# Performance work log

Hardware: AMD Instinct MI355X
Metric: run time of the kernel (lower is better)

The kernel has to match this reference:

```python
import jax, jax.numpy as jnp
import numpy as np

CHUNK = 1024  # rows of pc0 processed per tile to avoid materializing the full NxM matrix


def _min_sqdist(a, b):
    """For each row of a [N,3], min squared distance to rows of b [M,3]."""
    b_sq = jnp.sum(b * b, axis=1)  # [M]

    def tile_min(ac):  # ac: [CHUNK, 3]
        d = jnp.sum(ac * ac, axis=1)[:, None] + b_sq[None, :] - 2.0 * (ac @ b.T)
        return jnp.min(d, axis=1)

    n, dim = a.shape
    return jax.lax.map(tile_min, a.reshape(n // CHUNK, CHUNK, dim)).reshape(n)


def setup_inputs() -> dict:
    key = jax.random.key(0)
    k0, k1 = jax.random.split(key)
    pc0 = jax.random.normal(k0, (65536, 3), dtype=jnp.float32)
    pc1 = jax.random.normal(k1, (65536, 3), dtype=jnp.float32)
    return {"pc0": pc0, "pc1": pc1}


def reference(pc0, pc1):
    # chamfer forward: dist0[i] = min_j ||pc0[i]-pc1[j]||^2
    dist0 = _min_sqdist(pc0, pc1)
    mask = dist0 <= 2.0
    # mean over selected elements (boolean mask is constant wrt grads, as in torch)
    return jnp.sum(jnp.where(mask, dist0, 0.0)) / jnp.sum(mask).astype(dist0.dtype)
```

## Files before the change

### kernel.cpp

```cpp
#include <hip/hip_runtime.h>


constexpr int   NPTS  = 65536;
constexpr int   G     = 64;
constexpr int   NC    = G * G * G;
constexpr float H     = 0.125f;
constexpr float ORG   = -4.0f;
constexpr float INVH  = 8.0f;
constexpr int   G3    = 32;
constexpr float H3    = 0.25f;
constexpr float INVH3 = 4.0f;
constexpr int   BLOCK = 256;
constexpr int   PBLOCKS = 1024;
constexpr int   SB    = 128;
constexpr int   CHUNK = NC / SB;

__device__ __forceinline__ int cellOf(float x) {
  int c = (int)floorf((x - ORG) * INVH);
  return min(max(c, 0), G - 1);
}
__device__ __forceinline__ int cellOf3(float x) {
  int c = (int)floorf((x - ORG) * INVH3);
  return min(max(c, 0), G3 - 1);
}

__global__ __launch_bounds__(BLOCK) void count_kernel(
    const float* __restrict__ pc0, const float* __restrict__ pc1,
    unsigned* __restrict__ counts0, unsigned* __restrict__ counts1) {
  const int gid = blockIdx.x * BLOCK + threadIdx.x;
  const float* p; unsigned* cnt; int i;
  if (gid < NPTS) { p = pc1; cnt = counts1; i = gid; }
  else            { p = pc0; cnt = counts0; i = gid - NPTS; }
  const float x = p[3 * i], y = p[3 * i + 1], z = p[3 * i + 2];
  atomicAdd(&cnt[(cellOf(z) * G + cellOf(y)) * G + cellOf(x)], 1u);
}

__global__ __launch_bounds__(1024) void scan_partial_kernel(
    const unsigned* __restrict__ counts0, const unsigned* __restrict__ counts1,
    unsigned* __restrict__ partials) {
  const unsigned* counts = blockIdx.y ? counts0 : counts1;
  const int base = blockIdx.x * CHUNK + threadIdx.x * 2;
  unsigned sum = counts[base] + counts[base + 1];
  for (int o = 32; o; o >>= 1) sum += __shfl_down(sum, o, 64);
  __shared__ unsigned ws[16];
  if ((threadIdx.x & 63) == 0) ws[threadIdx.x >> 6] = sum;
  __syncthreads();
  if (threadIdx.x == 0) {
    unsigned t = 0;
    for (int w = 0; w < 16; ++w) t += ws[w];
    partials[blockIdx.y * SB + blockIdx.x] = t;
  }
}

__global__ __launch_bounds__(256) void scan_mid_kernel(
    unsigned* __restrict__ partials) {
  const int tid = threadIdx.x;
  const int g   = tid >> 7;
  const int li  = tid & 127;
  const unsigned v = partials[g * SB + li];
  unsigned inc = v;
  for (int o = 1; o < 64; o <<= 1) {
    const unsigned t = __shfl_up(inc, o, 64);
    if ((tid & 63) >= o) inc += t;
  }
  __shared__ unsigned wt[4];
  if ((tid & 63) == 63) wt[tid >> 6] = inc;
  __syncthreads();
  const unsigned woff = ((tid >> 6) & 1) ? wt[g << 1] : 0u;
  partials[g * SB + li] = woff + inc - v;
}

__global__ __launch_bounds__(1024) void scan_final_kernel(
    const unsigned* __restrict__ counts0, unsigned* __restrict__ cur0,
    const unsigned* __restrict__ counts1, unsigned* __restrict__ cur1,
    const unsigned* __restrict__ partials) {
  const unsigned* counts = blockIdx.y ? counts0 : counts1;
  unsigned* cur          = blockIdx.y ? cur0    : cur1;
  const int tid = threadIdx.x;
  const int base = blockIdx.x * CHUNK + tid * 2;
  const unsigned a = counts[base], b = counts[base + 1];
  const unsigned tsum = a + b;
  unsigned inc = tsum;
  for (int o = 1; o < 64; o <<= 1) {
    const unsigned t = __shfl_up(inc, o, 64);
    if ((tid & 63) >= o) inc += t;
  }
  __shared__ unsigned wt[16];
  if ((tid & 63) == 63) wt[tid >> 6] = inc;
  __syncthreads();
  if (tid < 16) {
    unsigned w = wt[tid];
    for (int o = 1; o < 16; o <<= 1) {
      const unsigned t = __shfl_up(w, o, 16);
      if (tid >= o) w += t;
    }
    wt[tid] = w;
  }
  __syncthreads();
  const unsigned woff = (tid >> 6) ? wt[(tid >> 6) - 1] : 0u;
  const unsigned off =
      partials[blockIdx.y * SB + blockIdx.x] + woff + inc - tsum;
  cur[base] = off;
  cur[base + 1] = off + a;
}

__global__ __launch_bounds__(BLOCK) void scatter_kernel(
    const float* __restrict__ pc0, const float* __restrict__ pc1,
    unsigned* __restrict__ cur0, unsigned* __restrict__ cur1,
    float4* __restrict__ q, float4* __restrict__ s) {
  const int gid = blockIdx.x * BLOCK + threadIdx.x;
  const float* p; unsigned* cur; float4* dst; int i;
  if (gid < NPTS) { p = pc1; cur = cur1; dst = s; i = gid; }
  else            { p = pc0; cur = cur0; dst = q; i = gid - NPTS; }
  const float x = p[3 * i], y = p[3 * i + 1], z = p[3 * i + 2];
  const int cid = (cellOf(z) * G + cellOf(y)) * G + cellOf(x);
  dst[atomicAdd(&cur[cid], 1u)] = make_float4(x, y, z, 0.f);
}

__global__ __launch_bounds__(BLOCK) void query_kernel(
    const float4* __restrict__ q, const unsigned* __restrict__ ends,
    const float4* __restrict__ s,
    unsigned* __restrict__ wl, float* __restrict__ wlBest,
    unsigned* __restrict__ pendCnt, float* __restrict__ bkt) {
  const int gtid = blockIdx.x * BLOCK + threadIdx.x;
  const int i   = gtid >> 2;
  const int sub = gtid & 3;
  const float4 p = q[i];
  const int cx = cellOf(p.x), cy = cellOf(p.y), cz = cellOf(p.z);
  const int x0 = max(cx - 1, 0), x1 = min(cx + 1, G - 1);

  unsigned rs[9], re[9];
#pragma unroll
  for (int rr = 0; rr < 9; ++rr) {
    const int zz = cz + rr / 3 - 1, yy = cy + rr % 3 - 1;
    const bool ok = (zz >= 0) && (zz < G) && (yy >= 0) && (yy < G);
    const int rb = ok ? (zz * G + yy) * G : 0;
    rs[rr] = ok ? ((rb + x0) ? ends[rb + x0 - 1] : 0u) : 0u;
    re[rr] = ok ? ends[rb + x1] : 0u;
  }
  float best = 3.4e38f;
#pragma unroll
  for (int rr = 0; rr < 9; ++rr) {
#pragma unroll 4
    for (unsigned j = rs[rr] + sub; j < re[rr]; j += 4) {
      const float4 c = s[j];
      const float dx = p.x - c.x, dy = p.y - c.y, dz = p.z - c.z;
      best = fminf(best, fmaf(dx, dx, fmaf(dy, dy, dz * dz)));
    }
  }
  best = fminf(best, __shfl_xor(best, 1, 64));
  best = fminf(best, __shfl_xor(best, 2, 64));

  float v = 0.f, c = 0.f;
  if (sub == 0) {
    const int y0 = max(cy - 1, 0), y1 = min(cy + 1, G - 1);
    const int z0 = max(cz - 1, 0), z1 = min(cz + 1, G - 1);
    const float dxl = (x0 == 0)     ? 1e9f : p.x - (ORG + (float)x0 * H);
    const float dxr = (x1 == G - 1) ? 1e9f : (ORG + (float)(x1 + 1) * H) - p.x;
    const float dyl = (y0 == 0)     ? 1e9f : p.y - (ORG + (float)y0 * H);
    const float dyr = (y1 == G - 1) ? 1e9f : (ORG + (float)(y1 + 1) * H) - p.y;
    const float dzl = (z0 == 0)     ? 1e9f : p.z - (ORG + (float)z0 * H);
    const float dzr = (z1 == G - 1) ? 1e9f : (ORG + (float)(z1 + 1) * H) - p.z;
    const float dbox = fminf(fminf(fminf(dxl, dxr), fminf(dyl, dyr)),
                             fminf(dzl, dzr));
    const float bnd2 = dbox * dbox * 0.999999f;
    if (best > bnd2) {
      const unsigned k = atomicAdd(pendCnt, 1u);
      wl[k] = (unsigned)i; wlBest[k] = best;
    } else if (best <= 2.0f) { v = best; c = 1.0f; }
  }

  for (int o = 32; o; o >>= 1) {
    v += __shfl_down(v, o, 64);
    c += __shfl_down(c, o, 64);
  }
  __shared__ float wsum[BLOCK / 64], wcnt[BLOCK / 64];
  const int wid = threadIdx.x >> 6;
  if ((threadIdx.x & 63) == 0) { wsum[wid] = v; wcnt[wid] = c; }
  __syncthreads();
  if (threadIdx.x == 0) {
    float bv = 0.f, bc = 0.f;
    for (int w = 0; w < BLOCK / 64; ++w) { bv += wsum[w]; bc += wcnt[w]; }
    if (bc != 0.f) {
      atomicAdd(&bkt[2 * (blockIdx.x & 63) + 0], bv);
      atomicAdd(&bkt[2 * (blockIdx.x & 63) + 1], bc);
    }
  }
}

__global__ __launch_bounds__(BLOCK) void pending_kernel(
    const float4* __restrict__ q,
    const unsigned* __restrict__ ends, const float4* __restrict__ s,
    const unsigned* __restrict__ wl, const float* __restrict__ wlBest,
    unsigned* __restrict__ pendCnt, float* __restrict__ bkt,
    unsigned* __restrict__ done, float* __restrict__ out) {
  __shared__ int snP;
  __shared__ float wsum[BLOCK / 64], wcnt[BLOCK / 64];
  __shared__ int isLast;
  __shared__ float fs[BLOCK / 64], fc[BLOCK / 64];
  if (threadIdx.x == 0) snP = (int)atomicAdd(pendCnt, 0u);
  __syncthreads();
  const int lane = threadIdx.x & 63, wid = threadIdx.x >> 6;
  const int gw = blockIdx.x * (BLOCK / 64) + wid;
  const int nW = PBLOCKS * (BLOCK / 64);
  float v = 0.f, c = 0.f;

  for (int it = gw; it < snP; it += nW) {
    const unsigned qi = wl[it];
    const float4 p = q[qi];
    const int cx = cellOf3(p.x), cy = cellOf3(p.y), cz = cellOf3(p.z);
    float best = wlBest[it];

    for (int r = 1; r <= 8; ++r) {
      const float cov = H3 * (float)(r - 1);
      if (best <= cov * cov) break;
      if (best > 2.0f && cov * cov >= 2.0f) break;
      const int S = (r == 1) ? 9 : 8 * r + 2 * (2 * r - 1) * (2 * r - 1);
      float b = best;
      for (int sI = lane; sI < S; sI += 64) {
        int dz, dy, xa, xb;
        if (r == 1) {
          dz = sI / 3 - 1; dy = sI % 3 - 1; xa = cx - 1; xb = cx + 1;
        } else if (sI < 8 * r) {
          if (sI < 2 * r + 1)      { dz = -r; dy = sI - r; }
          else if (sI < 4 * r + 2) { dz =  r; dy = sI - (2 * r + 1) - r; }
          else { const int t2 = sI - (4 * r + 2); dz = (t2 >> 1) - (r - 1);
                 dy = (t2 & 1) ? r : -r; }
          xa = cx - r; xb = cx + r;
        } else {
          const int t2 = sI - 8 * r, ci = t2 >> 1, w1 = 2 * r - 1;
          dz = ci / w1 - (r - 1); dy = ci % w1 - (r - 1);
          xa = xb = (t2 & 1) ? cx + r : cx - r;
        }
        const int Z = cz + dz, Y = cy + dy;
        if (Z < 0 || Z >= G3 || Y < 0 || Y >= G3) continue;
        int a3 = max(xa, 0), e3 = min(xb, G3 - 1);
        if (a3 > e3) continue;
        const float ylo = ORG + (float)Y * H3;
        const float zlo = ORG + (float)Z * H3;
        const float dyd = fmaxf(fmaxf(ylo - p.y, p.y - (ylo + H3)), 0.f);
        const float dzd = fmaxf(fmaxf(zlo - p.z, p.z - (zlo + H3)), 0.f);
        const float dyz2 = dyd * dyd + dzd * dzd;
        const float bnd = fminf(b, 2.0f);
        if (dyz2 >= bnd) continue;
        const float halfx = sqrtf(bnd - dyz2);
        const int xlo = (int)floorf((p.x - halfx - ORG) * INVH3);
        const int xhi = (int)floorf((p.x + halfx - ORG) * INVH3);
        a3 = max(a3, xlo); e3 = min(e3, xhi);
        if (a3 > e3) continue;
        const int xs = 2 * a3, xe = 2 * e3 + 1;
        unsigned js[4], je[4];
#pragma unroll
        for (int k = 0; k < 4; ++k) {
          const int zz = 2 * Z + (k >> 1), yy = 2 * Y + (k & 1);
          const int rb = (zz * G + yy) * G;
          js[k] = (rb + xs) ? ends[rb + xs - 1] : 0u;
          je[k] = ends[rb + xe];
        }
#pragma unroll
        for (int k = 0; k < 4; ++k) {
#pragma unroll 4
          for (unsigned j = js[k]; j < je[k]; ++j) {
            const float4 cd = s[j];
            const float dx = p.x - cd.x, dyv = p.y - cd.y, dzv = p.z - cd.z;
            b = fminf(b, fmaf(dx, dx, fmaf(dyv, dyv, dzv * dzv)));
          }
        }
      }
      for (int o = 32; o; o >>= 1) b = fminf(b, __shfl_xor(b, o, 64));
      best = b;
    }
    if (lane == 0 && best <= 2.0f) { v += best; c += 1.0f; }
  }

  if (lane == 0) { wsum[wid] = v; wcnt[wid] = c; }
  __syncthreads();
  if (threadIdx.x == 0) {
    float bv = 0.f, bc = 0.f;
    for (int w = 0; w < BLOCK / 64; ++w) { bv += wsum[w]; bc += wcnt[w]; }
    if (bc != 0.f) {
      atomicAdd(&bkt[2 * (blockIdx.x & 63) + 0], bv);
      atomicAdd(&bkt[2 * (blockIdx.x & 63) + 1], bc);
    }
    __threadfence();
    isLast = (atomicAdd(done, 1u) == (unsigned)(PBLOCKS - 1));
  }
  __syncthreads();
  if (isLast) {
    const float val = (threadIdx.x < 128) ? atomicAdd(&bkt[threadIdx.x], 0.0f) : 0.0f;
    float sv = (threadIdx.x & 1) ? 0.f : val;
    float cv = (threadIdx.x & 1) ? val : 0.f;
    for (int o = 32; o; o >>= 1) {
      sv += __shfl_down(sv, o, 64);
      cv += __shfl_down(cv, o, 64);
    }
    if (lane == 0) { fs[wid] = sv; fc[wid] = cv; }
    __syncthreads();
    if (threadIdx.x == 0) {
      float S = 0.f, C = 0.f;
      for (int w = 0; w < BLOCK / 64; ++w) { S += fs[w]; C += fc[w]; }
      out[0] = S / C;
    }
  }
}

extern "C" void kernel_launch(void* const* d_in, const int* in_sizes, int n_in,
                              void* d_out, int out_size, void* d_ws, size_t ws_size,
                              hipStream_t stream) {
  const float* pc0 = (const float*)d_in[0];
  const float* pc1 = (const float*)d_in[1];
  float* out = (float*)d_out;

  char* w = (char*)d_ws;
  auto nxt = [&](size_t bytes) {
    char* p = w; w += (bytes + 255) & ~(size_t)255; return p;
  };
  unsigned* counts1  = (unsigned*)nxt((size_t)NC * 4);
  unsigned* counts0  = (unsigned*)nxt((size_t)NC * 4);
  char*     misc     = nxt(1024);
  float*    bkt      = (float*)misc;
  unsigned* done     = (unsigned*)(misc + 512);
  unsigned* pendCnt  = (unsigned*)(misc + 516);
  unsigned* partials = (unsigned*)nxt((size_t)2 * SB * 4);
  unsigned* cur1     = (unsigned*)nxt((size_t)NC * 4);
  unsigned* cur0     = (unsigned*)nxt((size_t)NC * 4);
  float4*   s        = (float4*)nxt((size_t)NPTS * 16);
  float4*   q        = (float4*)nxt((size_t)NPTS * 16);
  unsigned* wl       = (unsigned*)nxt((size_t)NPTS * 4);
  float*    wlBest   = (float*)nxt((size_t)NPTS * 4);

  hipMemsetAsync(counts1, 0, (size_t)2 * NC * 4 + 1024, stream);

  count_kernel<<<2 * NPTS / BLOCK, BLOCK, 0, stream>>>(pc0, pc1, counts0, counts1);
  scan_partial_kernel<<<dim3(SB, 2), 1024, 0, stream>>>(counts0, counts1, partials);
  scan_mid_kernel<<<1, 256, 0, stream>>>(partials);
  scan_final_kernel<<<dim3(SB, 2), 1024, 0, stream>>>(counts0, cur0,
                                                      counts1, cur1, partials);
  scatter_kernel<<<2 * NPTS / BLOCK, BLOCK, 0, stream>>>(
      pc0, pc1, cur0, cur1, q, s);
  query_kernel<<<4 * NPTS / BLOCK, BLOCK, 0, stream>>>(q, cur1, s, wl, wlBest,
                                                       pendCnt, bkt);
  pending_kernel<<<PBLOCKS, BLOCK, 0, stream>>>(q, cur1, s, wl, wlBest,
                                                pendCnt, bkt, done, out);
}
```

Baseline: 136.6 us.

## Split each pending query's shell search across four wavefronts with atomic-min merge

Each pending query is now handled by four wavefronts instead of one. Each wavefront scans an interleaved quarter of the shell cells at every ring radius. Partial minima are merged with an atomicMin on the float's bit pattern, and the fourth wavefront to finish, detected through a per-query completion counter, adds the result to the masked sum. The aim is to cut the latency of long-running pending queries by adding parallelism, at the cost of extra atomics, a threadfence, a larger memset, and weaker early ring termination, since each subwave only sees its own running minimum.

```diff
diff --git a/kernel.cpp b/kernel.cpp
--- a/kernel.cpp
+++ b/kernel.cpp
@@ -12,6 +12,7 @@
 constexpr float INVH3 = 4.0f;
 constexpr int   BLOCK = 256;
 constexpr int   PBLOCKS = 1024;
+constexpr int   NSUB  = 4;
 constexpr int   SB    = 128;
 constexpr int   CHUNK = NC / SB;
 
@@ -26,8 +27,10 @@
 
 __global__ __launch_bounds__(BLOCK) void count_kernel(
     const float* __restrict__ pc0, const float* __restrict__ pc1,
-    unsigned* __restrict__ counts0, unsigned* __restrict__ counts1) {
+    unsigned* __restrict__ counts0, unsigned* __restrict__ counts1,
+    unsigned* __restrict__ pbestU) {
   const int gid = blockIdx.x * BLOCK + threadIdx.x;
+  if (gid < NPTS) pbestU[gid] = 0xFFFFFFFFu;
   const float* p; unsigned* cnt; int i;
   if (gid < NPTS) { p = pc1; cnt = counts1; i = gid; }
   else            { p = pc0; cnt = counts0; i = gid - NPTS; }
@@ -193,7 +196,8 @@
     const unsigned* __restrict__ ends, const float4* __restrict__ s,
     const unsigned* __restrict__ wl, const float* __restrict__ wlBest,
     unsigned* __restrict__ pendCnt, float* __restrict__ bkt,
-    unsigned* __restrict__ done, float* __restrict__ out) {
+    unsigned* __restrict__ done, float* __restrict__ out,
+    unsigned* __restrict__ pbestU, unsigned* __restrict__ pdone) {
   __shared__ int snP;
   __shared__ float wsum[BLOCK / 64], wcnt[BLOCK / 64];
   __shared__ int isLast;
@@ -205,7 +209,9 @@
   const int nW = PBLOCKS * (BLOCK / 64);
   float v = 0.f, c = 0.f;
 
-  for (int it = gw; it < snP; it += nW) {
+  for (int t = gw; t < snP * NSUB; t += nW) {
+    const int it  = t >> 2;
+    const int sw  = t & (NSUB - 1);
     const unsigned qi = wl[it];
     const float4 p = q[qi];
     const int cx = cellOf3(p.x), cy = cellOf3(p.y), cz = cellOf3(p.z);
@@ -217,7 +223,7 @@
       if (best > 2.0f && cov * cov >= 2.0f) break;
       const int S = (r == 1) ? 9 : 8 * r + 2 * (2 * r - 1) * (2 * r - 1);
       float b = best;
-      for (int sI = lane; sI < S; sI += 64) {
+      for (int sI = lane + (sw << 6); sI < S; sI += 64 * NSUB) {
         int dz, dy, xa, xb;
         if (r == 1) {
           dz = sI / 3 - 1; dy = sI % 3 - 1; xa = cx - 1; xb = cx + 1;
@@ -270,7 +276,14 @@
       for (int o = 32; o; o >>= 1) b = fminf(b, __shfl_xor(b, o, 64));
       best = b;
     }
-    if (lane == 0 && best <= 2.0f) { v += best; c += 1.0f; }
+    if (lane == 0) {
+      atomicMin(&pbestU[it], __float_as_uint(best));
+      __threadfence();
+      if (atomicAdd(&pdone[it], 1u) == NSUB - 1) {
+        const float fb = __uint_as_float(atomicAdd(&pbestU[it], 0u));
+        if (fb <= 2.0f) { v += fb; c += 1.0f; }
+      }
+    }
   }
 
   if (lane == 0) { wsum[wid] = v; wcnt[wid] = c; }
@@ -321,6 +334,7 @@
   float*    bkt      = (float*)misc;
   unsigned* done     = (unsigned*)(misc + 512);
   unsigned* pendCnt  = (unsigned*)(misc + 516);
+  unsigned* pdone    = (unsigned*)nxt((size_t)NPTS * 4);
   unsigned* partials = (unsigned*)nxt((size_t)2 * SB * 4);
   unsigned* cur1     = (unsigned*)nxt((size_t)NC * 4);
   unsigned* cur0     = (unsigned*)nxt((size_t)NC * 4);
@@ -328,10 +342,13 @@
   float4*   q        = (float4*)nxt((size_t)NPTS * 16);
   unsigned* wl       = (unsigned*)nxt((size_t)NPTS * 4);
   float*    wlBest   = (float*)nxt((size_t)NPTS * 4);
-
-  hipMemsetAsync(counts1, 0, (size_t)2 * NC * 4 + 1024, stream);
-
-  count_kernel<<<2 * NPTS / BLOCK, BLOCK, 0, stream>>>(pc0, pc1, counts0, counts1);
+  unsigned* pbestU   = (unsigned*)nxt((size_t)NPTS * 4);
+
+  hipMemsetAsync(counts1, 0, (size_t)2 * NC * 4 + 1024 + (size_t)NPTS * 4,
+                 stream);
+
+  count_kernel<<<2 * NPTS / BLOCK, BLOCK, 0, stream>>>(pc0, pc1, counts0,
+                                                       counts1, pbestU);
   scan_partial_kernel<<<dim3(SB, 2), 1024, 0, stream>>>(counts0, counts1, partials);
   scan_mid_kernel<<<1, 256, 0, stream>>>(partials);
   scan_final_kernel<<<dim3(SB, 2), 1024, 0, stream>>>(counts0, cur0,
@@ -341,5 +358,6 @@
   query_kernel<<<4 * NPTS / BLOCK, BLOCK, 0, stream>>>(q, cur1, s, wl, wlBest,
                                                        pendCnt, bkt);
   pending_kernel<<<PBLOCKS, BLOCK, 0, stream>>>(q, cur1, s, wl, wlBest,
-                                                pendCnt, bkt, done, out);
-}
+                                                pendCnt, bkt, done, out,
+                                                pbestU, pdone);
+}
```

New measurement: 348.7 us. 155% more time.

## Fuse query and pending kernels with a dynamic work-claiming queue

Applied to the files above, without the earlier changes.

Merges the first-pass query kernel and the pending-refinement kernel into one launch. Each block finishes its 3x3x3 cell query, publishes unresolved points to a worklist with fenced atomic writes, then its wavefronts claim worklist entries through an atomic counter. They spin with sleep until an entry is published or all query blocks are done. This removes a kernel launch and its tail gap, and lets refinement overlap with blocks still querying. In exchange it adds spin-wait polling, extra atomics, and a larger memset for the worklist tags.

```diff
diff --git a/kernel.cpp b/kernel.cpp
--- a/kernel.cpp
+++ b/kernel.cpp
@@ -11,7 +11,7 @@
 constexpr float H3    = 0.25f;
 constexpr float INVH3 = 4.0f;
 constexpr int   BLOCK = 256;
-constexpr int   PBLOCKS = 1024;
+constexpr int   NQB   = 4 * NPTS / BLOCK;
 constexpr int   SB    = 128;
 constexpr int   CHUNK = NC / SB;
 
@@ -117,99 +117,96 @@
   dst[atomicAdd(&cur[cid], 1u)] = make_float4(x, y, z, 0.f);
 }
 
-__global__ __launch_bounds__(BLOCK) void query_kernel(
+__global__ __launch_bounds__(BLOCK) void qp_kernel(
     const float4* __restrict__ q, const unsigned* __restrict__ ends,
     const float4* __restrict__ s,
-    unsigned* __restrict__ wl, float* __restrict__ wlBest,
-    unsigned* __restrict__ pendCnt, float* __restrict__ bkt) {
+    unsigned* __restrict__ wl, unsigned* __restrict__ wlBestU,
+    unsigned* __restrict__ pendCnt, unsigned* __restrict__ claim,
+    unsigned* __restrict__ qdone, float* __restrict__ bkt,
+    unsigned* __restrict__ done, float* __restrict__ out) {
   const int gtid = blockIdx.x * BLOCK + threadIdx.x;
-  const int i   = gtid >> 2;
-  const int sub = gtid & 3;
-  const float4 p = q[i];
-  const int cx = cellOf(p.x), cy = cellOf(p.y), cz = cellOf(p.z);
-  const int x0 = max(cx - 1, 0), x1 = min(cx + 1, G - 1);
-
-  unsigned rs[9], re[9];
+  const int lane = threadIdx.x & 63, wid = threadIdx.x >> 6;
+  float v = 0.f, c = 0.f;
+
+  {
+    const int i   = gtid >> 2;
+    const int sub = gtid & 3;
+    const float4 p = q[i];
+    const int cx = cellOf(p.x), cy = cellOf(p.y), cz = cellOf(p.z);
+    const int x0 = max(cx - 1, 0), x1 = min(cx + 1, G - 1);
+
+    unsigned rs[9], re[9];
 #pragma unroll
-  for (int rr = 0; rr < 9; ++rr) {
-    const int zz = cz + rr / 3 - 1, yy = cy + rr % 3 - 1;
-    const bool ok = (zz >= 0) && (zz < G) && (yy >= 0) && (yy < G);
-    const int rb = ok ? (zz * G + yy) * G : 0;
-    rs[rr] = ok ? ((rb + x0) ? ends[rb + x0 - 1] : 0u) : 0u;
-    re[rr] = ok ? ends[rb + x1] : 0u;
-  }
-  float best = 3.4e38f;
+    for (int rr = 0; rr < 9; ++rr) {
+      const int zz = cz + rr / 3 - 1, yy = cy + rr % 3 - 1;
+      const bool ok = (zz >= 0) && (zz < G) && (yy >= 0) && (yy < G);
+      const int rb = ok ? (zz * G + yy) * G : 0;
+      rs[rr] = ok ? ((rb + x0) ? ends[rb + x0 - 1] : 0u) : 0u;
+      re[rr] = ok ? ends[rb + x1] : 0u;
+    }
+    float best = 3.4e38f;
 #pragma unroll
-  for (int rr = 0; rr < 9; ++rr) {
+    for (int rr = 0; rr < 9; ++rr) {
 #pragma unroll 4
-    for (unsigned j = rs[rr] + sub; j < re[rr]; j += 4) {
-      const float4 c = s[j];
-      const float dx = p.x - c.x, dy = p.y - c.y, dz = p.z - c.z;
-      best = fminf(best, fmaf(dx, dx, fmaf(dy, dy, dz * dz)));
-    }
-  }
-  best = fminf(best, __shfl_xor(best, 1, 64));
-  best = fminf(best, __shfl_xor(best, 2, 64));
-
-  float v = 0.f, c = 0.f;
-  if (sub == 0) {
-    const int y0 = max(cy - 1, 0), y1 = min(cy + 1, G - 1);
-    const int z0 = max(cz - 1, 0), z1 = min(cz + 1, G - 1);
-    const float dxl = (x0 == 0)     ? 1e9f : p.x - (ORG + (float)x0 * H);
-    const float dxr = (x1 == G - 1) ? 1e9f : (ORG + (float)(x1 + 1) * H) - p.x;
-    const float dyl = (y0 == 0)     ? 1e9f : p.y - (ORG + (float)y0 * H);
-    const float dyr = (y1 == G - 1) ? 1e9f : (ORG + (float)(y1 + 1) * H) - p.y;
-    const float dzl = (z0 == 0)     ? 1e9f : p.z - (ORG + (float)z0 * H);
-    const float dzr = (z1 == G - 1) ? 1e9f : (ORG + (float)(z1 + 1) * H) - p.z;
-    const float dbox = fminf(fminf(fminf(dxl, dxr), fminf(dyl, dyr)),
-                             fminf(dzl, dzr));
-    const float bnd2 = dbox * dbox * 0.999999f;
-    if (best > bnd2) {
-      const unsigned k = atomicAdd(pendCnt, 1u);
-      wl[k] = (unsigned)i; wlBest[k] = best;
-    } else if (best <= 2.0f) { v = best; c = 1.0f; }
-  }
-
-  for (int o = 32; o; o >>= 1) {
-    v += __shfl_down(v, o, 64);
-    c += __shfl_down(c, o, 64);
-  }
-  __shared__ float wsum[BLOCK / 64], wcnt[BLOCK / 64];
-  const int wid = threadIdx.x >> 6;
-  if ((threadIdx.x & 63) == 0) { wsum[wid] = v; wcnt[wid] = c; }
-  __syncthreads();
-  if (threadIdx.x == 0) {
-    float bv = 0.f, bc = 0.f;
-    for (int w = 0; w < BLOCK / 64; ++w) { bv += wsum[w]; bc += wcnt[w]; }
-    if (bc != 0.f) {
-      atomicAdd(&bkt[2 * (blockIdx.x & 63) + 0], bv);
-      atomicAdd(&bkt[2 * (blockIdx.x & 63) + 1], bc);
-    }
-  }
-}
-
-__global__ __launch_bounds__(BLOCK) void pending_kernel(
-    const float4* __restrict__ q,
-    const unsigned* __restrict__ ends, const float4* __restrict__ s,
-    const unsigned* __restrict__ wl, const float* __restrict__ wlBest,
-    unsigned* __restrict__ pendCnt, float* __restrict__ bkt,
-    unsigned* __restrict__ done, float* __restrict__ out) {
-  __shared__ int snP;
-  __shared__ float wsum[BLOCK / 64], wcnt[BLOCK / 64];
-  __shared__ int isLast;
-  __shared__ float fs[BLOCK / 64], fc[BLOCK / 64];
-  if (threadIdx.x == 0) snP = (int)atomicAdd(pendCnt, 0u);
-  __syncthreads();
-  const int lane = threadIdx.x & 63, wid = threadIdx.x >> 6;
-  const int gw = blockIdx.x * (BLOCK / 64) + wid;
-  const int nW = PBLOCKS * (BLOCK / 64);
-  float v = 0.f, c = 0.f;
-
-  for (int it = gw; it < snP; it += nW) {
-    const unsigned qi = wl[it];
+      for (unsigned j = rs[rr] + sub; j < re[rr]; j += 4) {
+        const float4 cq = s[j];
+        const float dx = p.x - cq.x, dy = p.y - cq.y, dz = p.z - cq.z;
+        best = fminf(best, fmaf(dx, dx, fmaf(dy, dy, dz * dz)));
+      }
+    }
+    best = fminf(best, __shfl_xor(best, 1, 64));
+    best = fminf(best, __shfl_xor(best, 2, 64));
+
+    if (sub == 0) {
+      const int y0 = max(cy - 1, 0), y1 = min(cy + 1, G - 1);
+      const int z0 = max(cz - 1, 0), z1 = min(cz + 1, G - 1);
+      const float dxl = (x0 == 0)     ? 1e9f : p.x - (ORG + (float)x0 * H);
+      const float dxr = (x1 == G - 1) ? 1e9f : (ORG + (float)(x1 + 1) * H) - p.x;
+      const float dyl = (y0 == 0)     ? 1e9f : p.y - (ORG + (float)y0 * H);
+      const float dyr = (y1 == G - 1) ? 1e9f : (ORG + (float)(y1 + 1) * H) - p.y;
+      const float dzl = (z0 == 0)     ? 1e9f : p.z - (ORG + (float)z0 * H);
+      const float dzr = (z1 == G - 1) ? 1e9f : (ORG + (float)(z1 + 1) * H) - p.z;
+      const float dbox = fminf(fminf(fminf(dxl, dxr), fminf(dyl, dyr)),
+                               fminf(dzl, dzr));
+      const float bnd2 = dbox * dbox * 0.999999f;
+      if (best > bnd2) {
+        const unsigned k = atomicAdd(pendCnt, 1u);
+        atomicExch(&wlBestU[k], __float_as_uint(best));
+        __threadfence();
+        atomicExch(&wl[k], (unsigned)i + 1u);
+      } else if (best <= 2.0f) { v = best; c = 1.0f; }
+    }
+  }
+  __syncthreads();
+  if (threadIdx.x == 0) { __threadfence(); atomicAdd(qdone, 1u); }
+
+  for (;;) {
+    unsigned k = 0;
+    if (lane == 0) k = atomicAdd(claim, 1u);
+    k = __shfl(k, 0, 64);
+    if (k >= (unsigned)NPTS) break;
+    unsigned tag = 0;
+    if (lane == 0) {
+      int sp = 0;
+      for (;;) {
+        tag = atomicAdd(&wl[k], 0u);
+        if (tag) break;
+        if ((++sp & 3) == 0 &&
+            atomicAdd(qdone, 0u) == (unsigned)NQB &&
+            atomicAdd(pendCnt, 0u) <= k) break;
+        __builtin_amdgcn_s_sleep(15);
+      }
+    }
+    tag = __shfl(tag, 0, 64);
+    if (!tag) break;
+    unsigned bU = 0;
+    if (lane == 0) { __threadfence(); bU = atomicAdd(&wlBestU[k], 0u); }
+    bU = __shfl(bU, 0, 64);
+
+    const unsigned qi = tag - 1u;
     const float4 p = q[qi];
     const int cx = cellOf3(p.x), cy = cellOf3(p.y), cz = cellOf3(p.z);
-    float best = wlBest[it];
+    float best = __uint_as_float(bU);
 
     for (int r = 1; r <= 8; ++r) {
       const float cov = H3 * (float)(r - 1);
@@ -251,16 +248,16 @@
         const int xs = 2 * a3, xe = 2 * e3 + 1;
         unsigned js[4], je[4];
 #pragma unroll
-        for (int k = 0; k < 4; ++k) {
-          const int zz = 2 * Z + (k >> 1), yy = 2 * Y + (k & 1);
+        for (int k2 = 0; k2 < 4; ++k2) {
+          const int zz = 2 * Z + (k2 >> 1), yy = 2 * Y + (k2 & 1);
           const int rb = (zz * G + yy) * G;
-          js[k] = (rb + xs) ? ends[rb + xs - 1] : 0u;
-          je[k] = ends[rb + xe];
+          js[k2] = (rb + xs) ? ends[rb + xs - 1] : 0u;
+          je[k2] = ends[rb + xe];
         }
 #pragma unroll
-        for (int k = 0; k < 4; ++k) {
+        for (int k2 = 0; k2 < 4; ++k2) {
 #pragma unroll 4
-          for (unsigned j = js[k]; j < je[k]; ++j) {
+          for (unsigned j = js[k2]; j < je[k2]; ++j) {
             const float4 cd = s[j];
             const float dx = p.x - cd.x, dyv = p.y - cd.y, dzv = p.z - cd.z;
             b = fminf(b, fmaf(dx, dx, fmaf(dyv, dyv, dzv * dzv)));
@@ -273,17 +270,23 @@
     if (lane == 0 && best <= 2.0f) { v += best; c += 1.0f; }
   }
 
-  if (lane == 0) { wsum[wid] = v; wcnt[wid] = c; }
+  for (int o = 32; o; o >>= 1) {
+    v += __shfl_down(v, o, 64);
+    c += __shfl_down(c, o, 64);
+  }
+  __shared__ float fs[BLOCK / 64], fc[BLOCK / 64];
+  __shared__ int isLast;
+  if (lane == 0) { fs[wid] = v; fc[wid] = c; }
   __syncthreads();
   if (threadIdx.x == 0) {
     float bv = 0.f, bc = 0.f;
-    for (int w = 0; w < BLOCK / 64; ++w) { bv += wsum[w]; bc += wcnt[w]; }
+    for (int w = 0; w < BLOCK / 64; ++w) { bv += fs[w]; bc += fc[w]; }
     if (bc != 0.f) {
       atomicAdd(&bkt[2 * (blockIdx.x & 63) + 0], bv);
       atomicAdd(&bkt[2 * (blockIdx.x & 63) + 1], bc);
     }
     __threadfence();
-    isLast = (atomicAdd(done, 1u) == (unsigned)(PBLOCKS - 1));
+    isLast = (atomicAdd(done, 1u) == (unsigned)(NQB - 1));
   }
   __syncthreads();
   if (isLast) {
@@ -294,6 +297,7 @@
       sv += __shfl_down(sv, o, 64);
       cv += __shfl_down(cv, o, 64);
     }
+    __syncthreads();
     if (lane == 0) { fs[wid] = sv; fc[wid] = cv; }
     __syncthreads();
     if (threadIdx.x == 0) {
@@ -321,15 +325,18 @@
   float*    bkt      = (float*)misc;
   unsigned* done     = (unsigned*)(misc + 512);
   unsigned* pendCnt  = (unsigned*)(misc + 516);
+  unsigned* claim    = (unsigned*)(misc + 520);
+  unsigned* qdone    = (unsigned*)(misc + 524);
+  unsigned* wl       = (unsigned*)nxt((size_t)NPTS * 4);
   unsigned* partials = (unsigned*)nxt((size_t)2 * SB * 4);
   unsigned* cur1     = (unsigned*)nxt((size_t)NC * 4);
   unsigned* cur0     = (unsigned*)nxt((size_t)NC * 4);
   float4*   s        = (float4*)nxt((size_t)NPTS * 16);
   float4*   q        = (float4*)nxt((size_t)NPTS * 16);
-  unsigned* wl       = (unsigned*)nxt((size_t)NPTS * 4);
-  float*    wlBest   = (float*)nxt((size_t)NPTS * 4);
-
-  hipMemsetAsync(counts1, 0, (size_t)2 * NC * 4 + 1024, stream);
+  unsigned* wlBestU  = (unsigned*)nxt((size_t)NPTS * 4);
+
+  hipMemsetAsync(counts1, 0, (size_t)2 * NC * 4 + 1024 + (size_t)NPTS * 4,
+                 stream);
 
   count_kernel<<<2 * NPTS / BLOCK, BLOCK, 0, stream>>>(pc0, pc1, counts0, counts1);
   scan_partial_kernel<<<dim3(SB, 2), 1024, 0, stream>>>(counts0, counts1, partials);
@@ -338,8 +345,6 @@
                                                       counts1, cur1, partials);
   scatter_kernel<<<2 * NPTS / BLOCK, BLOCK, 0, stream>>>(
       pc0, pc1, cur0, cur1, q, s);
-  query_kernel<<<4 * NPTS / BLOCK, BLOCK, 0, stream>>>(q, cur1, s, wl, wlBest,
-                                                       pendCnt, bkt);
-  pending_kernel<<<PBLOCKS, BLOCK, 0, stream>>>(q, cur1, s, wl, wlBest,
-                                                pendCnt, bkt, done, out);
-}
+  qp_kernel<<<NQB, BLOCK, 0, stream>>>(q, cur1, s, wl, wlBestU,
+                                       pendCnt, claim, qdone, bkt, done, out);
+}
```

Measured after the change: 452.9 us. 231% more time.
